# Optimization experiments

Measured on AMD Instinct MI355X. Metric: run time of the kernel, lower is better.

The kernel has to match this reference:

```python
import jax, jax.numpy as jnp
import numpy as np

BN_EPS = 1e-5


def setup_inputs() -> dict:
    key = jax.random.key(0)
    k1, k2 = jax.random.split(key)
    B, IN, OUT = 16384, 2048, 2048
    x = jax.random.normal(k1, (B, IN), dtype=jnp.float32)
    weight = jax.random.normal(k2, (OUT, IN), dtype=jnp.float32) * 0.05
    gamma = jnp.ones((OUT,), dtype=jnp.float32)
    beta = jnp.zeros((OUT,), dtype=jnp.float32)
    return {"x": x, "weight": weight, "gamma": gamma, "beta": beta}


def reference(x, weight, gamma, beta):
    # Deterministic binarization: sign(w) in {-1, +1} (0 maps to +1)
    w_bin = jnp.where(weight >= 0, 1.0, -1.0).astype(weight.dtype)
    # Linear (no bias): y = x @ W_bin^T  -> [B, OUT]
    y = jnp.einsum("bi,oi->bo", x, w_bin)
    # BatchNorm1d, training mode: biased batch statistics over batch dim
    mean = jnp.mean(y, axis=0)
    var = jnp.mean(jnp.square(y - mean), axis=0)
    y = (y - mean) * (gamma * jax.lax.rsqrt(var + BN_EPS)) + beta
    # ReLU activation
    return jax.nn.relu(y)
```

## Files before the change

### kernel.cpp

```cpp
#include <hip/hip_runtime.h>
#include <stdint.h>

#define B_DIM   16384
#define IN_DIM  2048
#define OUT_DIM 2048
#define BN_EPS  1e-5f

typedef int    i32x4 __attribute__((ext_vector_type(4)));
typedef unsigned short u16x4 __attribute__((ext_vector_type(4)));


__device__ __forceinline__ unsigned short f2bf_rne(float f) {
    unsigned u = __builtin_bit_cast(unsigned, f);
    return (unsigned short)((u + 0x7fffu + ((u >> 16) & 1u)) >> 16);
}
__device__ __forceinline__ float bf2f(unsigned short h) {
    unsigned u = ((unsigned)h) << 16;
    return __builtin_bit_cast(float, u);
}

__device__ __forceinline__ void gl_lds16(const void* g, void* l) {
    __builtin_amdgcn_global_load_lds(
        (const __attribute__((address_space(1))) unsigned int*)g,
        (__attribute__((address_space(3))) unsigned int*)l,
        16, 0, 0);
}

__device__ __forceinline__ int pack4(float a, float b, float c, float d, float inv) {
    int q0 = (int)rintf(a * inv) & 255;
    int q1 = (int)rintf(b * inv) & 255;
    int q2 = (int)rintf(c * inv) & 255;
    int q3 = (int)rintf(d * inv) & 255;
    return q0 | (q1 << 8) | (q2 << 16) | (q3 << 24);
}

__global__ __launch_bounds__(256) void quantize_x_kernel(
        const float4* __restrict__ x4, int* __restrict__ xq,
        float* __restrict__ scales) {
    __shared__ float wmax[4];
    const int row = blockIdx.x;
    const int t = threadIdx.x;
    const float4* xr = x4 + (size_t)row * 512;
    float4 a = xr[t];
    float4 b = xr[t + 256];
    float m = fmaxf(fmaxf(fabsf(a.x), fabsf(a.y)), fmaxf(fabsf(a.z), fabsf(a.w)));
    m = fmaxf(m, fmaxf(fmaxf(fabsf(b.x), fabsf(b.y)), fmaxf(fabsf(b.z), fabsf(b.w))));
#pragma unroll
    for (int off = 32; off >= 1; off >>= 1) m = fmaxf(m, __shfl_xor(m, off));
    if ((t & 63) == 0) wmax[t >> 6] = m;
    __syncthreads();
    m = fmaxf(fmaxf(wmax[0], wmax[1]), fmaxf(wmax[2], wmax[3]));
    m = fmaxf(m, 1e-20f);
    const float inv = 127.0f / m;
    if (t == 0) scales[row] = m * (1.0f / 127.0f);
    int* xo = xq + (size_t)row * 512;
    xo[t]       = pack4(a.x, a.y, a.z, a.w, inv);
    xo[t + 256] = pack4(b.x, b.y, b.z, b.w, inv);
}

__global__ __launch_bounds__(256) void convert_w_kernel(
        const float4* __restrict__ w, int* __restrict__ wq,
        float4* __restrict__ stats ) {
    int id = blockIdx.x * 256 + threadIdx.x;
    if (id < 1024) stats[id] = make_float4(0.f, 0.f, 0.f, 0.f);
    float4 a = w[id];
    int b0 = (a.x < 0.f) ? 0xFF : 0x01;
    int b1 = (a.y < 0.f) ? 0xFF : 0x01;
    int b2 = (a.z < 0.f) ? 0xFF : 0x01;
    int b3 = (a.w < 0.f) ? 0xFF : 0x01;
    wq[id] = b0 | (b1 << 8) | (b2 << 16) | (b3 << 24);
}

__global__ __launch_bounds__(512, 2) void gemm_bn_kernel(
        const char* __restrict__ A, const char* __restrict__ Bw,
        const float* __restrict__ scales,
        unsigned short* __restrict__ Yb,
        float* __restrict__ colsum, float* __restrict__ colsumsq) {
    __shared__ __align__(16) char smem[131072];

    const int tid  = threadIdx.x;
    const int wave = tid >> 6;
    const int lane = tid & 63;
    const int wm = wave >> 2;
    const int wn = wave & 3;
    const int lr = lane & 15;
    const int lq = lane >> 4;

    const int b  = blockIdx.x;
    const int lb = (b & 7) * 64 + (b >> 3);
    const int bm = (lb >> 3) * 256;
    const int bn = (lb & 7) * 256;

    const int swz16 = (((tid & 7) ^ ((tid >> 3) & 7)) << 4);
    const char* gA = A  + (size_t)(bm + (tid >> 3)) * IN_DIM + swz16;
    const char* gB = Bw + (size_t)(bn + (tid >> 3)) * IN_DIM + swz16;
    const int ldst = tid << 4;

    const int aRd = wm * 16384 + lr * 128;
    const int bRd = wn * 8192  + lr * 128;
    const int sl0 = ((lq    ) ^ (lr & 7)) << 4;
    const int sl1 = ((lq + 4) ^ (lr & 7)) << 4;

    i32x4 acc[8][4];
#pragma unroll
    for (int i = 0; i < 8; ++i)
#pragma unroll
        for (int j = 0; j < 4; ++j) {
            i32x4 z = {0, 0, 0, 0};
            acc[i][j] = z;
        }

#define VM_WAIT(N) asm volatile("s_waitcnt vmcnt(" #N ")" ::: "memory")
#define LGKM0()    asm volatile("s_waitcnt lgkmcnt(0)" ::: "memory")
#define BAR()      __builtin_amdgcn_s_barrier()

#define MM16(IB) \
    _Pragma("unroll") for (int i = 0; i < 4; ++i) \
    _Pragma("unroll") for (int j = 0; j < 4; ++j) \
        acc[(IB) + i][j] = __builtin_amdgcn_mfma_i32_16x16x64_i8( \
            av[i], bv[j], acc[(IB) + i][j], 0, 0, 0)

    {
        char* An = smem;
        char* Bn = smem + 32768;
        gl_lds16(gB + 0 * 131072, Bn + 0 * 8192 + ldst);
        gl_lds16(gB + 1 * 131072, Bn + 1 * 8192 + ldst);
        gl_lds16(gB + 2 * 131072, Bn + 2 * 8192 + ldst);
        gl_lds16(gB + 3 * 131072, Bn + 3 * 8192 + ldst);
        gl_lds16(gA + 0 * 131072, An + 0 * 8192 + ldst);
        gl_lds16(gA + 2 * 131072, An + 2 * 8192 + ldst);
        gl_lds16(gA + 1 * 131072, An + 1 * 8192 + ldst);
        gl_lds16(gA + 3 * 131072, An + 3 * 8192 + ldst);
        VM_WAIT(2);
        BAR();
    }

#define GTILE(t_, LAST_) do {                                                  \
    const char* Ab = smem + (((t_) & 1) ? 65536 : 0);                          \
    const char* Bb = Ab + 32768;                                               \
    char* An = smem + (((t_) & 1) ? 0 : 65536);                                \
    char* Bn = An + 32768;                                                     \
    const size_t kn = (size_t)((t_) + 1) * 128;                                \
    i32x4 av[4], bv[4];                                                        \
                        \
    _Pragma("unroll") for (int j = 0; j < 4; ++j)                              \
        bv[j] = *(const i32x4*)(Bb + bRd + j * 2048 + sl0);                    \
    _Pragma("unroll") for (int i = 0; i < 4; ++i)                              \
        av[i] = *(const i32x4*)(Ab + aRd + i * 2048 + sl0);                    \
    if (!(LAST_)) {                                                            \
        gl_lds16(gB + kn          , Bn + 0 * 8192 + ldst);                     \
        gl_lds16(gB + kn + 131072 , Bn + 1 * 8192 + ldst);                     \
        gl_lds16(gB + kn + 262144 , Bn + 2 * 8192 + ldst);                     \
        gl_lds16(gB + kn + 393216 , Bn + 3 * 8192 + ldst);                     \
    }                                                                          \
    if (LAST_) { VM_WAIT(0); } else { VM_WAIT(4); }       \
    BAR(); LGKM0();                                                            \
    __builtin_amdgcn_s_setprio(1);                                             \
    MM16(0);                                                                   \
    __builtin_amdgcn_s_setprio(0);                                             \
    BAR();                                                                     \
                   \
    _Pragma("unroll") for (int i = 0; i < 4; ++i)                              \
        av[i] = *(const i32x4*)(Ab + aRd + (i + 4) * 2048 + sl0);              \
    if (!(LAST_)) {                                                            \
        gl_lds16(gA + kn          , An + 0 * 8192 + ldst);                     \
        gl_lds16(gA + kn + 262144 , An + 2 * 8192 + ldst);                     \
        gl_lds16(gA + kn + 131072 , An + 1 * 8192 + ldst);                     \
        gl_lds16(gA + kn + 393216 , An + 3 * 8192 + ldst);                     \
    }                                                                          \
    BAR(); LGKM0();                                                            \
    __builtin_amdgcn_s_setprio(1);                                             \
    MM16(4);                                                                   \
    __builtin_amdgcn_s_setprio(0);                                             \
    BAR();                                                                     \
                               \
    _Pragma("unroll") for (int j = 0; j < 4; ++j)                              \
        bv[j] = *(const i32x4*)(Bb + bRd + j * 2048 + sl1);                    \
    _Pragma("unroll") for (int i = 0; i < 4; ++i)                              \
        av[i] = *(const i32x4*)(Ab + aRd + i * 2048 + sl1);                    \
    BAR(); LGKM0();                                                            \
    __builtin_amdgcn_s_setprio(1);                                             \
    MM16(0);                                                                   \
    __builtin_amdgcn_s_setprio(0);                                             \
    BAR();                                                                     \
      \
    _Pragma("unroll") for (int i = 0; i < 4; ++i)                              \
        av[i] = *(const i32x4*)(Ab + aRd + (i + 4) * 2048 + sl1);              \
    VM_WAIT(2);                                                                \
    BAR(); LGKM0();                                                            \
    __builtin_amdgcn_s_setprio(1);                                             \
    MM16(4);                                                                   \
    __builtin_amdgcn_s_setprio(0);                                             \
    BAR();                                                                     \
} while (0)

    for (int t = 0; t < 15; ++t) GTILE(t, 0);
    GTILE(15, 1);

#undef GTILE
#undef MM16
#undef VM_WAIT
#undef LGKM0
#undef BAR

    float colS[4], colQ[4];
#pragma unroll
    for (int j = 0; j < 4; ++j) { colS[j] = 0.f; colQ[j] = 0.f; }

#pragma unroll
    for (int i = 0; i < 8; ++i) {
        const int row0 = bm + wm * 128 + i * 16 + lq * 4;
        float sc[4];
#pragma unroll
        for (int r = 0; r < 4; ++r) sc[r] = scales[row0 + r];
#pragma unroll
        for (int r = 0; r < 4; ++r) {
            size_t base = (size_t)(row0 + r) * OUT_DIM + bn + wn * 64 + lr;
#pragma unroll
            for (int j = 0; j < 4; ++j) {
                float v = (float)acc[i][j][r] * sc[r];
                Yb[base + j * 16] = f2bf_rne(v);
                colS[j] += v;
                colQ[j] += v * v;
            }
        }
    }

#pragma unroll
    for (int j = 0; j < 4; ++j) {
        float s = colS[j], q = colQ[j];
        s += __shfl_xor(s, 16); s += __shfl_xor(s, 32);
        q += __shfl_xor(q, 16); q += __shfl_xor(q, 32);
        if (lq == 0) {
            int col = bn + wn * 64 + j * 16 + lr;
            atomicAdd(&colsum[col], s);
            atomicAdd(&colsumsq[col], q);
        }
    }
}

__global__ __launch_bounds__(256) void finalize_kernel(
        const float* __restrict__ colsum, const float* __restrict__ colsumsq,
        const float* __restrict__ gamma, const float* __restrict__ beta,
        float* __restrict__ scale, float* __restrict__ bias) {
    int n = blockIdx.x * 256 + threadIdx.x;
    if (n < OUT_DIM) {
        const float inv = 1.f / (float)B_DIM;
        float mean = colsum[n] * inv;
        float var  = colsumsq[n] * inv - mean * mean;
        float sc   = gamma[n] * rsqrtf(var + BN_EPS);
        scale[n] = sc;
        bias[n]  = beta[n] - mean * sc;
    }
}

__global__ __launch_bounds__(256) void bn_relu_bf16_kernel(
        const u16x4* __restrict__ yb, float4* __restrict__ out,
        const float4* __restrict__ scale4, const float4* __restrict__ bias4) {
    int base = blockIdx.x * 512 + threadIdx.x;
#pragma unroll
    for (int p = 0; p < 2; ++p) {
        int id = base + p * 256;
        int c4 = id & (OUT_DIM / 4 - 1);
        u16x4 h = yb[id];
        float4 s = scale4[c4];
        float4 bb = bias4[c4];
        float4 v;
        v.x = fmaxf(fmaf(bf2f(h[0]), s.x, bb.x), 0.f);
        v.y = fmaxf(fmaf(bf2f(h[1]), s.y, bb.y), 0.f);
        v.z = fmaxf(fmaf(bf2f(h[2]), s.z, bb.z), 0.f);
        v.w = fmaxf(fmaf(bf2f(h[3]), s.w, bb.w), 0.f);
        out[id] = v;
    }
}

extern "C" void kernel_launch(void* const* d_in, const int* in_sizes, int n_in,
                              void* d_out, int out_size, void* d_ws, size_t ws_size,
                              hipStream_t stream) {
    const float* x     = (const float*)d_in[0];
    const float* w     = (const float*)d_in[1];
    const float* gamma = (const float*)d_in[2];
    const float* beta  = (const float*)d_in[3];
    float* out = (float*)d_out;

    char* ws = (char*)d_ws;
    const size_t XQ_OFF = 0;
    const size_t WQ_OFF = XQ_OFF + (size_t)B_DIM * IN_DIM;
    const size_t YB_OFF = WQ_OFF + (size_t)OUT_DIM * IN_DIM;
    const size_t ST_OFF = YB_OFF + (size_t)B_DIM * OUT_DIM * 2;
    const size_t SC_OFF = ST_OFF + 8192 * 4;

    char* xq = ws + XQ_OFF;
    char* wq = ws + WQ_OFF;
    unsigned short* yb = (unsigned short*)(ws + YB_OFF);
    float* colsum   = (float*)(ws + ST_OFF);
    float* colsumsq = colsum + 2048;
    float* scale    = colsum + 4096;
    float* bias     = colsum + 6144;
    float* scales   = (float*)(ws + SC_OFF);

    quantize_x_kernel<<<B_DIM, 256, 0, stream>>>(
        (const float4*)x, (int*)xq, scales);
    convert_w_kernel<<<4096, 256, 0, stream>>>(
        (const float4*)w, (int*)wq, (float4*)colsum);
    gemm_bn_kernel<<<512, 512, 0, stream>>>(
        xq, wq, scales, yb, colsum, colsumsq);
    finalize_kernel<<<8, 256, 0, stream>>>(
        colsum, colsumsq, gamma, beta, scale, bias);
    bn_relu_bf16_kernel<<<16384, 256, 0, stream>>>(
        (const u16x4*)yb, (float4*)out, (const float4*)scale,
        (const float4*)bias);
}
```

Before: 328.7 us.

## Switch int8 GEMM from 16x16x64 to 32x32x32 MFMA tiles

```diff
diff --git a/kernel.cpp b/kernel.cpp
--- a/kernel.cpp
+++ b/kernel.cpp
@@ -6,7 +6,8 @@
 #define OUT_DIM 2048
 #define BN_EPS  1e-5f
 
-typedef int    i32x4 __attribute__((ext_vector_type(4)));
+typedef int    i32x4  __attribute__((ext_vector_type(4)));
+typedef int    i32x16 __attribute__((ext_vector_type(16)));
 typedef unsigned short u16x4 __attribute__((ext_vector_type(4)));
 
 
@@ -83,8 +84,8 @@
     const int lane = tid & 63;
     const int wm = wave >> 2;
     const int wn = wave & 3;
-    const int lr = lane & 15;
-    const int lq = lane >> 4;
+    const int l31 = lane & 31;
+    const int hi  = lane >> 5;
 
     const int b  = blockIdx.x;
     const int lb = (b & 7) * 64 + (b >> 3);
@@ -96,29 +97,30 @@
     const char* gB = Bw + (size_t)(bn + (tid >> 3)) * IN_DIM + swz16;
     const int ldst = tid << 4;
 
-    const int aRd = wm * 16384 + lr * 128;
-    const int bRd = wn * 8192  + lr * 128;
-    const int sl0 = ((lq    ) ^ (lr & 7)) << 4;
-    const int sl1 = ((lq + 4) ^ (lr & 7)) << 4;
-
-    i32x4 acc[8][4];
-#pragma unroll
-    for (int i = 0; i < 8; ++i)
-#pragma unroll
-        for (int j = 0; j < 4; ++j) {
-            i32x4 z = {0, 0, 0, 0};
-            acc[i][j] = z;
-        }
+    const int sw   = l31 & 7;
+    const int aRd  = (wm * 128 + l31) * 128;
+    const int bRd  = 32768 + (wn * 64 + l31) * 128;
+
+    i32x16 acc[4][2];
+#pragma unroll
+    for (int i = 0; i < 4; ++i)
+#pragma unroll
+        for (int j = 0; j < 2; ++j)
+            acc[i][j] = (i32x16)(0);
 
 #define VM_WAIT(N) asm volatile("s_waitcnt vmcnt(" #N ")" ::: "memory")
 #define LGKM0()    asm volatile("s_waitcnt lgkmcnt(0)" ::: "memory")
 #define BAR()      __builtin_amdgcn_s_barrier()
-
-#define MM16(IB) \
-    _Pragma("unroll") for (int i = 0; i < 4; ++i) \
-    _Pragma("unroll") for (int j = 0; j < 4; ++j) \
-        acc[(IB) + i][j] = __builtin_amdgcn_mfma_i32_16x16x64_i8( \
-            av[i], bv[j], acc[(IB) + i][j], 0, 0, 0)
+#define ACHUNK(kf_) ((((kf_) * 2 + hi) ^ sw) << 4)
+#define ARD(Ab_, i_, kf_) (*(const i32x4*)((Ab_) + aRd + (i_) * 4096 + ACHUNK(kf_)))
+#define BRD(Ab_, j_, kf_) (*(const i32x4*)((Ab_) + bRd + (j_) * 4096 + ACHUNK(kf_)))
+
+#define MM8(I0) \
+    _Pragma("unroll") for (int ii = 0; ii < 2; ++ii) \
+    _Pragma("unroll") for (int jj = 0; jj < 2; ++jj) \
+    _Pragma("unroll") for (int ff = 0; ff < 2; ++ff) \
+        acc[(I0) + ii][jj] = __builtin_amdgcn_mfma_i32_32x32x32_i8( \
+            av[ii][ff], bv[jj][ff], acc[(I0) + ii][jj], 0, 0, 0)
 
     {
         char* An = smem;
@@ -137,16 +139,17 @@
 
 #define GTILE(t_, LAST_) do {                                                  \
     const char* Ab = smem + (((t_) & 1) ? 65536 : 0);                          \
-    const char* Bb = Ab + 32768;                                               \
     char* An = smem + (((t_) & 1) ? 0 : 65536);                                \
     char* Bn = An + 32768;                                                     \
     const size_t kn = (size_t)((t_) + 1) * 128;                                \
-    i32x4 av[4], bv[4];                                                        \
-                        \
-    _Pragma("unroll") for (int j = 0; j < 4; ++j)                              \
-        bv[j] = *(const i32x4*)(Bb + bRd + j * 2048 + sl0);                    \
-    _Pragma("unroll") for (int i = 0; i < 4; ++i)                              \
-        av[i] = *(const i32x4*)(Ab + aRd + i * 2048 + sl0);                    \
+    i32x4 av[2][2], bv[2][2];                                                  \
+                   \
+    _Pragma("unroll") for (int jj = 0; jj < 2; ++jj)                           \
+    _Pragma("unroll") for (int ff = 0; ff < 2; ++ff)                           \
+        bv[jj][ff] = BRD(Ab, jj, ff);                                          \
+    _Pragma("unroll") for (int ii = 0; ii < 2; ++ii)                           \
+    _Pragma("unroll") for (int ff = 0; ff < 2; ++ff)                           \
+        av[ii][ff] = ARD(Ab, ii, ff);                                          \
     if (!(LAST_)) {                                                            \
         gl_lds16(gB + kn          , Bn + 0 * 8192 + ldst);                     \
         gl_lds16(gB + kn + 131072 , Bn + 1 * 8192 + ldst);                     \
@@ -156,12 +159,13 @@
     if (LAST_) { VM_WAIT(0); } else { VM_WAIT(4); }       \
     BAR(); LGKM0();                                                            \
     __builtin_amdgcn_s_setprio(1);                                             \
-    MM16(0);                                                                   \
+    MM8(0);                                                                    \
     __builtin_amdgcn_s_setprio(0);                                             \
     BAR();                                                                     \
-                   \
-    _Pragma("unroll") for (int i = 0; i < 4; ++i)                              \
-        av[i] = *(const i32x4*)(Ab + aRd + (i + 4) * 2048 + sl0);              \
+              \
+    _Pragma("unroll") for (int ii = 0; ii < 2; ++ii)                           \
+    _Pragma("unroll") for (int ff = 0; ff < 2; ++ff)                           \
+        av[ii][ff] = ARD(Ab, ii + 2, ff);                                      \
     if (!(LAST_)) {                                                            \
         gl_lds16(gA + kn          , An + 0 * 8192 + ldst);                     \
         gl_lds16(gA + kn + 262144 , An + 2 * 8192 + ldst);                     \
@@ -170,26 +174,29 @@
     }                                                                          \
     BAR(); LGKM0();                                                            \
     __builtin_amdgcn_s_setprio(1);                                             \
-    MM16(4);                                                                   \
+    MM8(2);                                                                    \
     __builtin_amdgcn_s_setprio(0);                                             \
     BAR();                                                                     \
-                               \
-    _Pragma("unroll") for (int j = 0; j < 4; ++j)                              \
-        bv[j] = *(const i32x4*)(Bb + bRd + j * 2048 + sl1);                    \
-    _Pragma("unroll") for (int i = 0; i < 4; ++i)                              \
-        av[i] = *(const i32x4*)(Ab + aRd + i * 2048 + sl1);                    \
+                          \
+    _Pragma("unroll") for (int jj = 0; jj < 2; ++jj)                           \
+    _Pragma("unroll") for (int ff = 0; ff < 2; ++ff)                           \
+        bv[jj][ff] = BRD(Ab, jj, ff + 2);                                      \
+    _Pragma("unroll") for (int ii = 0; ii < 2; ++ii)                           \
+    _Pragma("unroll") for (int ff = 0; ff < 2; ++ff)                           \
+        av[ii][ff] = ARD(Ab, ii, ff + 2);                                      \
     BAR(); LGKM0();                                                            \
     __builtin_amdgcn_s_setprio(1);                                             \
-    MM16(0);                                                                   \
+    MM8(0);                                                                    \
     __builtin_amdgcn_s_setprio(0);                                             \
     BAR();                                                                     \
-      \
-    _Pragma("unroll") for (int i = 0; i < 4; ++i)                              \
-        av[i] = *(const i32x4*)(Ab + aRd + (i + 4) * 2048 + sl1);              \
+       \
+    _Pragma("unroll") for (int ii = 0; ii < 2; ++ii)                           \
+    _Pragma("unroll") for (int ff = 0; ff < 2; ++ff)                           \
+        av[ii][ff] = ARD(Ab, ii + 2, ff + 2);                                  \
     VM_WAIT(2);                                                                \
     BAR(); LGKM0();                                                            \
     __builtin_amdgcn_s_setprio(1);                                             \
-    MM16(4);                                                                   \
+    MM8(2);                                                                    \
     __builtin_amdgcn_s_setprio(0);                                             \
     BAR();                                                                     \
 } while (0)
@@ -198,28 +205,29 @@
     GTILE(15, 1);
 
 #undef GTILE
-#undef MM16
+#undef MM8
+#undef ARD
+#undef BRD
+#undef ACHUNK
 #undef VM_WAIT
 #undef LGKM0
 #undef BAR
 
-    float colS[4], colQ[4];
-#pragma unroll
-    for (int j = 0; j < 4; ++j) { colS[j] = 0.f; colQ[j] = 0.f; }
-
-#pragma unroll
-    for (int i = 0; i < 8; ++i) {
-        const int row0 = bm + wm * 128 + i * 16 + lq * 4;
-        float sc[4];
-#pragma unroll
-        for (int r = 0; r < 4; ++r) sc[r] = scales[row0 + r];
-#pragma unroll
-        for (int r = 0; r < 4; ++r) {
-            size_t base = (size_t)(row0 + r) * OUT_DIM + bn + wn * 64 + lr;
-#pragma unroll
-            for (int j = 0; j < 4; ++j) {
-                float v = (float)acc[i][j][r] * sc[r];
-                Yb[base + j * 16] = f2bf_rne(v);
+    float colS[2], colQ[2];
+#pragma unroll
+    for (int j = 0; j < 2; ++j) { colS[j] = 0.f; colQ[j] = 0.f; }
+
+#pragma unroll
+    for (int i = 0; i < 4; ++i) {
+#pragma unroll
+        for (int r = 0; r < 16; ++r) {
+            const int row = bm + wm * 128 + i * 32 + (r & 3) + 8 * (r >> 2) + 4 * hi;
+            const float sc = scales[row];
+            const size_t base = (size_t)row * OUT_DIM + bn + wn * 64 + l31;
+#pragma unroll
+            for (int j = 0; j < 2; ++j) {
+                float v = (float)acc[i][j][r] * sc;
+                Yb[base + j * 32] = f2bf_rne(v);
                 colS[j] += v;
                 colQ[j] += v * v;
             }
@@ -227,12 +235,12 @@
     }
 
 #pragma unroll
-    for (int j = 0; j < 4; ++j) {
+    for (int j = 0; j < 2; ++j) {
         float s = colS[j], q = colQ[j];
-        s += __shfl_xor(s, 16); s += __shfl_xor(s, 32);
-        q += __shfl_xor(q, 16); q += __shfl_xor(q, 32);
-        if (lq == 0) {
-            int col = bn + wn * 64 + j * 16 + lr;
+        s += __shfl_xor(s, 32);
+        q += __shfl_xor(q, 32);
+        if (hi == 0) {
+            int col = bn + wn * 64 + j * 32 + l31;
             atomicAdd(&colsum[col], s);
             atomicAdd(&colsumsq[col], q);
         }
```

After: 329.9 us. No clear change (+0.4%).
